# Performance work log

Hardware: AMD Instinct MI355X
Metric: run time of the kernel (lower is better)

## Reference

```python
import jax, jax.numpy as jnp
import numpy as np

NUM_GROUPS = 8
EPS = 1e-5


def group_norm(x, gamma, beta):
    # x: [B, C, H, W], groups over channel dim
    b, c, h, w = x.shape
    xg = x.reshape(b, NUM_GROUPS, c // NUM_GROUPS, h, w)
    mean = xg.mean(axis=(2, 3, 4), keepdims=True)
    var = xg.var(axis=(2, 3, 4), keepdims=True)
    xg = (xg - mean) * jax.lax.rsqrt(var + EPS)
    x = xg.reshape(b, c, h, w)
    return x * gamma[None, :, None, None] + beta[None, :, None, None]


def conv1x1(x, w, bias):
    # 1x1 conv == per-pixel linear: [B,C,H,W] x [O,C] -> [B,O,H,W]
    return jnp.einsum('bchw,oc->bohw', x, w) + bias[None, :, None, None]


def setup_inputs() -> dict:
    key = jax.random.key(0)
    ks = jax.random.split(key, 6)
    B, C, H, W = 16, 512, 32, 32
    s = 1.0 / np.sqrt(C)  # conv2d default init scale-ish
    return {
        'x': jax.random.normal(ks[0], (B, C, H, W), jnp.float32),
        'gn_w': jnp.ones((C,), jnp.float32),
        'gn_b': jnp.zeros((C,), jnp.float32),
        'wq': jax.random.normal(ks[1], (C, C), jnp.float32) * s,
        'bq': jnp.zeros((C,), jnp.float32),
        'wk': jax.random.normal(ks[2], (C, C), jnp.float32) * s,
        'bk': jnp.zeros((C,), jnp.float32),
        'wv': jax.random.normal(ks[3], (C, C), jnp.float32) * s,
        'bv': jnp.zeros((C,), jnp.float32),
        'wo': jax.random.normal(ks[4], (C, C), jnp.float32) * s,
        'bo': jnp.zeros((C,), jnp.float32),
    }


def reference(x, gn_w, gn_b, wq, bq, wk, bk, wv, bv, wo, bo):
    b, c, h, w = x.shape
    scale = c ** (-0.5)
    hn = group_norm(x, gn_w, gn_b)
    q = conv1x1(hn, wq, bq).reshape(b, c, h * w).transpose(0, 2, 1)  # [B, N, C]
    k = conv1x1(hn, wk, bk).reshape(b, c, h * w).transpose(0, 2, 1)  # [B, N, C]
    v = conv1x1(hn, wv, bv).reshape(b, c, h * w).transpose(0, 2, 1)  # [B, N, C]
    attn = jnp.einsum('bnc,bmc->bnm', q, k) * scale                 # [B, N, N]
    attn = jax.nn.softmax(attn, axis=-1)
    out = jnp.einsum('bnm,bmc->bnc', attn, v)                       # [B, N, C]
    out = out.transpose(0, 2, 1).reshape(b, c, h, w)
    out = conv1x1(out, wo, bo)
    return x + out
```

## Files before the change

### kernel.cpp

```cpp
#include <hip/hip_runtime.h>
#include <stdint.h>

#define C_DIM 512
#define HW_N  1024
#define CPG   64
#define EPS_GN 1e-5f
#define SCALE_QK 0.044194173824159216f

typedef __attribute__((ext_vector_type(8))) __bf16 bf16x8v;
typedef __attribute__((ext_vector_type(4))) float  f32x4;

typedef __attribute__((address_space(1))) void gvoid_t;
typedef __attribute__((address_space(3))) void lvoid_t;

__device__ __forceinline__ void gload_lds16(const void* g, void* l) {
  __builtin_amdgcn_global_load_lds((gvoid_t*)g, (lvoid_t*)l, 16, 0, 0);
}

__device__ __forceinline__ uint16_t f2bfbits(float f) {
  __bf16 h = (__bf16)f;
  return __builtin_bit_cast(uint16_t, h);
}

__device__ __forceinline__ float bf2f(uint16_t u) {
  return __builtin_bit_cast(float, (uint32_t)u << 16);
}

template<int N>
__device__ __forceinline__ void vm_wait() {
  if constexpr (N == 0) asm volatile("s_waitcnt vmcnt(0)" ::: "memory");
  else if constexpr (N == 3) asm volatile("s_waitcnt vmcnt(3)" ::: "memory");
  else asm volatile("s_waitcnt vmcnt(4)" ::: "memory");
}

__global__ __launch_bounds__(256)
void gn_stats(const float* __restrict__ x, float2* __restrict__ part)
{
  const int lin  = blockIdx.x;
  const int b    = lin >> 4;
  const int g    = (lin >> 1) & 7;
  const int half = lin & 1;
  const int t    = threadIdx.x;

  const float4* xv = (const float4*)(x + ((long long)(b * C_DIM + g * CPG)) * HW_N
                                       + half * 512);
  float s1 = 0.f, s2 = 0.f;
  for (int i = t; i < 64 * 128; i += 256) {
    const int c  = i >> 7;
    const int nf = i & 127;
    float4 v = xv[c * 256 + nf];
    s1 += v.x + v.y + v.z + v.w;
    s2 += v.x * v.x + v.y * v.y + v.z * v.z + v.w * v.w;
  }
  #pragma unroll
  for (int off = 32; off; off >>= 1) {
    s1 += __shfl_xor(s1, off);
    s2 += __shfl_xor(s2, off);
  }
  __shared__ float red[2][4];
  const int w = t >> 6, l = t & 63;
  if (l == 0) { red[0][w] = s1; red[1][w] = s2; }
  __syncthreads();
  if (t == 0) {
    s1 = red[0][0] + red[0][1] + red[0][2] + red[0][3];
    s2 = red[1][0] + red[1][1] + red[1][2] + red[1][3];
    part[lin] = make_float2(s1, s2);
  }
}

__global__ __launch_bounds__(512)
void gn_norm(const float* __restrict__ x, const float2* __restrict__ part,
             const float* __restrict__ gnw, const float* __restrict__ gnb,
             __bf16* __restrict__ hn)
{
  const int b  = blockIdx.x >> 4;
  const int nc = blockIdx.x & 15;
  const int t  = threadIdx.x;

  __shared__ float asc[512], bsc[512];
  __shared__ float tile[64][65];

  {
    const int c = t;
    const int g = c >> 6;
    float2 p0 = part[(b * 8 + g) * 2 + 0];
    float2 p1 = part[(b * 8 + g) * 2 + 1];
    const float mean = (p0.x + p1.x) * (1.f / 65536.f);
    const float var  = (p0.y + p1.y) * (1.f / 65536.f) - mean * mean;
    const float rstd = rsqrtf(var + EPS_GN);
    const float a = rstd * gnw[c];
    asc[c] = a;
    bsc[c] = gnb[c] - mean * a;
  }
  __syncthreads();

  const long long xb = (long long)b * C_DIM * HW_N + nc * 64;
  __bf16* ob = hn + ((long long)b * HW_N + nc * 64) * C_DIM;

  for (int cg = 0; cg < 8; ++cg) {
    #pragma unroll
    for (int pass = 0; pass < 2; ++pass) {
      const int task = pass * 512 + t;
      const int c  = task >> 4;
      const int f4 = task & 15;
      float4 v = *(const float4*)(x + xb + (long long)(cg * 64 + c) * HW_N + f4 * 4);
      const float a  = asc[cg * 64 + c];
      const float bb = bsc[cg * 64 + c];
      tile[c][f4 * 4 + 0] = v.x * a + bb;
      tile[c][f4 * 4 + 1] = v.y * a + bb;
      tile[c][f4 * 4 + 2] = v.z * a + bb;
      tile[c][f4 * 4 + 3] = v.w * a + bb;
    }
    __syncthreads();
    {
      const int n  = t >> 3;
      const int gc = t & 7;
      uint32_t p[4];
      #pragma unroll
      for (int j = 0; j < 4; ++j) {
        const float f0 = tile[gc * 8 + 2 * j + 0][n];
        const float f1 = tile[gc * 8 + 2 * j + 1][n];
        p[j] = (uint32_t)f2bfbits(f0) | ((uint32_t)f2bfbits(f1) << 16);
      }
      *(uint4*)(ob + (long long)n * C_DIM + cg * 64 + gc * 8) =
          make_uint4(p[0], p[1], p[2], p[3]);
    }
    __syncthreads();
  }
}

__global__ __launch_bounds__(256)
void prep_kernel(const float* __restrict__ wq, const float* __restrict__ wk,
                 const float* __restrict__ wv, const float* __restrict__ wo,
                 const float* __restrict__ bq, const float* __restrict__ bk,
                 __bf16* __restrict__ wqkb, __bf16* __restrict__ wvb,
                 __bf16* __restrict__ wob, float* __restrict__ bqk)
{
  const int blk = blockIdx.x;
  if (blk < 1024) {
    const int which = blk >> 8;
    const int i = (blk & 255) * 256 + threadIdx.x;
    const float* src = (which == 0) ? wq : (which == 1) ? wk : (which == 2) ? wv : wo;
    __bf16* dst = (which == 0) ? wqkb
               : (which == 1) ? (wqkb + (size_t)C_DIM * C_DIM)
               : (which == 2) ? wvb : wob;
    const float scale = (which == 0) ? SCALE_QK : 1.f;
    float4 v = ((const float4*)src)[i];
    uint32_t lo = (uint32_t)f2bfbits(v.x * scale) | ((uint32_t)f2bfbits(v.y * scale) << 16);
    uint32_t hi = (uint32_t)f2bfbits(v.z * scale) | ((uint32_t)f2bfbits(v.w * scale) << 16);
    ((uint2*)dst)[i] = make_uint2(lo, hi);
  } else {
    for (int j = threadIdx.x; j < 1024; j += 256)
      bqk[j] = (j < 512) ? bq[j] * SCALE_QK : bk[j - 512];
  }
}

__global__ __launch_bounds__(256)
void softmax_kernel(__bf16* __restrict__ S)
{
  const long long row = blockIdx.x;
  uint2* sp = (uint2*)(S + row * HW_N);
  const int t = threadIdx.x;
  uint2 raw = sp[t];
  float v0 = bf2f((uint16_t)(raw.x & 0xffff));
  float v1 = bf2f((uint16_t)(raw.x >> 16));
  float v2 = bf2f((uint16_t)(raw.y & 0xffff));
  float v3 = bf2f((uint16_t)(raw.y >> 16));
  float m = fmaxf(fmaxf(v0, v1), fmaxf(v2, v3));
  #pragma unroll
  for (int off = 32; off; off >>= 1) m = fmaxf(m, __shfl_xor(m, off));
  __shared__ float redm[4];
  __shared__ float reds[4];
  const int w = t >> 6, l = t & 63;
  if (l == 0) redm[w] = m;
  __syncthreads();
  m = fmaxf(fmaxf(redm[0], redm[1]), fmaxf(redm[2], redm[3]));
  float e0 = __expf(v0 - m), e1 = __expf(v1 - m);
  float e2 = __expf(v2 - m), e3 = __expf(v3 - m);
  float sum = e0 + e1 + e2 + e3;
  #pragma unroll
  for (int off = 32; off; off >>= 1) sum += __shfl_xor(sum, off);
  if (l == 0) reds[w] = sum;
  __syncthreads();
  sum = reds[0] + reds[1] + reds[2] + reds[3];
  const float inv = 1.f / sum;
  uint32_t lo = (uint32_t)f2bfbits(e0 * inv) | ((uint32_t)f2bfbits(e1 * inv) << 16);
  uint32_t hi = (uint32_t)f2bfbits(e2 * inv) | ((uint32_t)f2bfbits(e3 * inv) << 16);
  sp[t] = make_uint2(lo, hi);
}

template<int BM, int OUTM, int BIASM>
__global__ __launch_bounds__(512, 2)
void gemm8(const __bf16* __restrict__ Amat, const __bf16* __restrict__ Bmat,
           void* __restrict__ Cmat,
           const float* __restrict__ bias,
           const float* __restrict__ resid,
           int lda, int ldb, int ldc,
           long long aS, long long bS, long long cS, int K)
{
  constexpr int TILE_B = BM * 64 + 16384;
  constexpr int CA = BM / 128;
  constexpr int CH = CA + 2;
  constexpr int FPR = BM / 32;
  constexpr int FPP = FPR / 2;

  __shared__ alignas(16) char lds[3 * TILE_B];

  const int tt = threadIdx.x;
  const int w  = tt >> 6;
  const int l  = tt & 63;
  const int lr = l & 15;
  const int lg = l >> 4;
  const int wm = w >> 2;
  const int wn = w & 3;
  const int b  = blockIdx.z;
  const int n0 = blockIdx.x * 256;
  const int m0 = blockIdx.y * BM;

  const __bf16* Ab = Amat + (long long)b * aS;
  const __bf16* Bb = Bmat + (long long)b * bS;

  const int srow = tt >> 2;
  const int sgr  = (tt & 3) ^ ((tt >> 3) & 3);

  f32x4 acc[FPR][4];
  #pragma unroll
  for (int f = 0; f < FPR; ++f)
    #pragma unroll
    for (int c = 0; c < 4; ++c)
      acc[f][c] = (f32x4){0.f, 0.f, 0.f, 0.f};

  auto stage = [&](int t, int c) {
    const int k0 = t << 5;
    char* dst = lds + (t % 3) * TILE_B + c * 8192 + w * 1024;
    const __bf16* src;
    if (c < CA) src = Ab + (long long)(m0 + c * 128 + srow) * lda + k0 + sgr * 8;
    else        src = Bb + (long long)(n0 + (c - CA) * 128 + srow) * ldb + k0 + sgr * 8;
    gload_lds16(src, dst);
  };
  auto rdA = [&](const char* base, int f) -> bf16x8v {
    const int row = wm * (BM / 2) + f * 16 + lr;
    return *(const bf16x8v*)(base + row * 64 + ((lg ^ ((row >> 1) & 3)) << 4));
  };
  auto rdB = [&](const char* base, int c) -> bf16x8v {
    const int row = wn * 64 + c * 16 + lr;
    return *(const bf16x8v*)(base + BM * 64 + row * 64 + ((lg ^ ((row >> 1) & 3)) << 4));
  };

  const int NT = K >> 5;

  #pragma unroll
  for (int c = 0; c < CH; ++c) stage(0, c);
  #pragma unroll
  for (int c = 0; c < CH; ++c) stage(1, c);

  for (int t = 0; t < NT; ++t) {
    const char* buf = lds + (t % 3) * TILE_B;
    if (t + 1 < NT) vm_wait<CH>();
    else            vm_wait<0>();
    __builtin_amdgcn_s_barrier();
    __builtin_amdgcn_sched_barrier(0);

    bf16x8v Bf[4];
    #pragma unroll
    for (int c = 0; c < 4; ++c) Bf[c] = rdB(buf, c);
    bf16x8v Af[FPP];
    #pragma unroll
    for (int f = 0; f < FPP; ++f) Af[f] = rdA(buf, f);
    if (t + 2 < NT) { stage(t + 2, 0); stage(t + 2, 1); }
    asm volatile("s_waitcnt lgkmcnt(0)" ::: "memory");
    __builtin_amdgcn_sched_barrier(0);
    __builtin_amdgcn_s_setprio(1);
    #pragma unroll
    for (int f = 0; f < FPP; ++f)
      #pragma unroll
      for (int c = 0; c < 4; ++c)
        acc[f][c] = __builtin_amdgcn_mfma_f32_16x16x32_bf16(Af[f], Bf[c], acc[f][c], 0, 0, 0);
    __builtin_amdgcn_s_setprio(0);
    __builtin_amdgcn_s_barrier();
    __builtin_amdgcn_sched_barrier(0);

    bf16x8v Ag[FPP];
    #pragma unroll
    for (int f = 0; f < FPP; ++f) Ag[f] = rdA(buf, FPP + f);
    if (t + 2 < NT) {
      #pragma unroll
      for (int c = 2; c < CH; ++c) stage(t + 2, c);
    }
    asm volatile("s_waitcnt lgkmcnt(0)" ::: "memory");
    __builtin_amdgcn_sched_barrier(0);
    __builtin_amdgcn_s_setprio(1);
    #pragma unroll
    for (int f = 0; f < FPP; ++f)
      #pragma unroll
      for (int c = 0; c < 4; ++c)
        acc[FPP + f][c] = __builtin_amdgcn_mfma_f32_16x16x32_bf16(Ag[f], Bf[c], acc[FPP + f][c], 0, 0, 0);
    __builtin_amdgcn_s_setprio(0);
    __builtin_amdgcn_s_barrier();
    __builtin_amdgcn_sched_barrier(0);
  }

  #pragma unroll
  for (int f = 0; f < FPR; ++f) {
    const int rrb = m0 + wm * (BM / 2) + f * 16 + lg * 4;
    #pragma unroll
    for (int c = 0; c < 4; ++c) {
      const int cc = n0 + wn * 64 + c * 16 + lr;
      const float cbias = (BIASM == 1) ? bias[cc] : 0.f;
      #pragma unroll
      for (int r = 0; r < 4; ++r) {
        const int rr = rrb + r;
        float v = acc[f][c][r];
        if (BIASM == 1) v += cbias;
        if (BIASM == 2) v += bias[rr];
        const long long idx = (long long)rr * ldc + cc;
        if (OUTM == 0) {
          ((__bf16*)Cmat + (long long)b * cS)[idx] = (__bf16)v;
        } else if (OUTM == 2) {
          ((float*)Cmat + (long long)b * cS)[idx] = v;
        } else {
          float* Cf = (float*)Cmat + (long long)b * cS;
          const float* Rf = resid + (long long)b * cS;
          Cf[idx] = v + Rf[idx];
        }
      }
    }
  }
}

extern "C" void kernel_launch(void* const* d_in, const int* in_sizes, int n_in,
                              void* d_out, int out_size, void* d_ws, size_t ws_size,
                              hipStream_t stream)
{
  const float* x   = (const float*)d_in[0];
  const float* gnw = (const float*)d_in[1];
  const float* gnb = (const float*)d_in[2];
  const float* wq  = (const float*)d_in[3];
  const float* bq  = (const float*)d_in[4];
  const float* wk  = (const float*)d_in[5];
  const float* bk  = (const float*)d_in[6];
  const float* wv  = (const float*)d_in[7];
  const float* bv  = (const float*)d_in[8];
  const float* wo  = (const float*)d_in[9];
  const float* bo  = (const float*)d_in[10];
  (void)in_sizes; (void)n_in; (void)out_size; (void)ws_size;

  size_t used = 0;
  char* base = (char*)d_ws;
  auto carve = [&](size_t bytes) -> void* {
    used = (used + 255) & ~(size_t)255;
    void* p = base + used;
    used += bytes;
    return p;
  };

  __bf16* wqkb = (__bf16*)carve((size_t)2 * C_DIM * C_DIM * 2);
  __bf16* wvb  = (__bf16*)carve((size_t)C_DIM * C_DIM * 2);
  __bf16* wob  = (__bf16*)carve((size_t)C_DIM * C_DIM * 2);
  float*  bqk  = (float*) carve((size_t)1024 * 4);
  float2* part = (float2*)carve((size_t)256 * 8);

  __bf16* hn   = (__bf16*)carve((size_t)16 * HW_N * C_DIM * 2);
  __bf16* qkb  = (__bf16*)carve((size_t)16 * HW_N * 1024 * 2);
  __bf16* vtb  = (__bf16*)carve((size_t)16 * C_DIM * HW_N * 2);
  __bf16* o1b  = (__bf16*)carve((size_t)16 * HW_N * C_DIM * 2);
  __bf16* Sb   = (__bf16*)carve((size_t)16 * HW_N * HW_N * 2);

  const long long sNC = (long long)HW_N * C_DIM;
  const long long sNN = (long long)HW_N * 1024;

  prep_kernel<<<dim3(1025), 256, 0, stream>>>(wq, wk, wv, wo, bq, bk,
                                              wqkb, wvb, wob, bqk);
  gn_stats<<<dim3(256), 256, 0, stream>>>(x, part);
  gn_norm<<<dim3(256), 512, 0, stream>>>(x, part, gnw, gnb, hn);

  gemm8<256, 0, 1><<<dim3(4, 4, 16), 512, 0, stream>>>(hn, wqkb, qkb, bqk, nullptr,
      C_DIM, C_DIM, 1024, sNC, 0, sNN, C_DIM);

  gemm8<128, 0, 2><<<dim3(4, 4, 16), 512, 0, stream>>>(wvb, hn, vtb, bv, nullptr,
      C_DIM, C_DIM, HW_N, 0, sNC, sNC, C_DIM);

  gemm8<256, 0, 0><<<dim3(4, 4, 16), 512, 0, stream>>>(qkb, qkb + 512, Sb, nullptr, nullptr,
      1024, 1024, 1024, sNN, sNN, sNN, C_DIM);

  softmax_kernel<<<dim3(16 * 1024), 256, 0, stream>>>(Sb);

  gemm8<128, 0, 0><<<dim3(2, 8, 16), 512, 0, stream>>>(Sb, vtb, o1b,
      nullptr, nullptr, 1024, 1024, C_DIM, sNN, sNC, sNC, HW_N);

  gemm8<128, 1, 2><<<dim3(4, 4, 16), 512, 0, stream>>>(wob, o1b, (float*)d_out, bo, x,
      C_DIM, C_DIM, HW_N, 0, sNC, sNC, C_DIM);
}
```

Baseline: 158.3 us.

## Add 256x256 double-buffered quadrant-pipelined GEMM kernel for bf16-output GEMMs

Adds a new gemm256 kernel that computes a 256x256 output tile per 512-thread block. It uses two LDS buffers of 64 KB each and splits every k-step into four quadrant MFMA phases, with the global-to-LDS stages for the next tiles interleaved between phases. The QK projection, V projection, QK^T scores and attention-times-V GEMMs switch to it, so the V and PV launches become larger tiles on fewer blocks. The goal is more arithmetic intensity and better overlap of loads with MFMA, at the cost of 128 KB LDS per block (occupancy risk) and fewer blocks for two of the GEMMs.

```diff
diff --git a/kernel.cpp b/kernel.cpp
--- a/kernel.cpp
+++ b/kernel.cpp
@@ -28,9 +28,10 @@
 
 template<int N>
 __device__ __forceinline__ void vm_wait() {
-  if constexpr (N == 0) asm volatile("s_waitcnt vmcnt(0)" ::: "memory");
+  if constexpr (N == 0)      asm volatile("s_waitcnt vmcnt(0)" ::: "memory");
   else if constexpr (N == 3) asm volatile("s_waitcnt vmcnt(3)" ::: "memory");
-  else asm volatile("s_waitcnt vmcnt(4)" ::: "memory");
+  else if constexpr (N == 4) asm volatile("s_waitcnt vmcnt(4)" ::: "memory");
+  else if constexpr (N == 6) asm volatile("s_waitcnt vmcnt(6)" ::: "memory");
 }
 
 __global__ __launch_bounds__(256)
@@ -189,6 +190,164 @@
   sp[t] = make_uint2(lo, hi);
 }
 
+#define QMFMA(QA, QB, BREG)                                                    \
+  do {                                                                         \
+    __builtin_amdgcn_s_setprio(1);                                             \
+    _Pragma("unroll")                                                          \
+    for (int f_ = 0; f_ < 4; ++f_)                                             \
+      _Pragma("unroll")                                                        \
+      for (int c_ = 0; c_ < 2; ++c_)                                           \
+        _Pragma("unroll")                                                      \
+        for (int kk_ = 0; kk_ < 2; ++kk_)                                      \
+          acc[QA][QB][f_][c_] = __builtin_amdgcn_mfma_f32_16x16x32_bf16(       \
+              Ar[f_][kk_], BREG[c_][kk_], acc[QA][QB][f_][c_], 0, 0, 0);       \
+    __builtin_amdgcn_s_setprio(0);                                             \
+  } while (0)
+
+#define LGKM0_FENCE()                                                          \
+  asm volatile("s_waitcnt lgkmcnt(0)" ::: "memory");                           \
+  __builtin_amdgcn_sched_barrier(0)
+
+template<int BIASM>
+__global__ __launch_bounds__(512, 2)
+void gemm256(const __bf16* __restrict__ Amat, const __bf16* __restrict__ Bmat,
+             __bf16* __restrict__ Cmat, const float* __restrict__ bias,
+             int lda, int ldb, int ldc,
+             long long aS, long long bS, long long cS, int K)
+{
+  __shared__ alignas(16) char lds[131072];
+
+  const int tt = threadIdx.x;
+  const int w  = tt >> 6;
+  const int l  = tt & 63;
+  const int lr = l & 15;
+  const int lg = l >> 4;
+  const int wm = w >> 2;
+  const int wn = w & 3;
+  const int b  = blockIdx.z;
+  const int n0 = blockIdx.x * 256;
+  const int m0 = blockIdx.y * 256;
+
+  const __bf16* Ab = Amat + (long long)b * aS;
+  const __bf16* Bb = Bmat + (long long)b * bS;
+
+  const int r0  = tt >> 3;
+  const int sg8 = ((tt & 7) ^ ((tt >> 3) & 7)) << 3;
+
+  f32x4 acc[2][2][4][2];
+  #pragma unroll
+  for (int qa = 0; qa < 2; ++qa)
+    #pragma unroll
+    for (int qb = 0; qb < 2; ++qb)
+      #pragma unroll
+      for (int f = 0; f < 4; ++f)
+        #pragma unroll
+        for (int c = 0; c < 2; ++c)
+          acc[qa][qb][f][c] = (f32x4){0.f, 0.f, 0.f, 0.f};
+
+  auto stage = [&](int kt, int h) {
+    char* dst = lds + ((kt & 1) << 16) + (h << 14) + w * 1024;
+    const long long ld = (h < 2) ? lda : ldb;
+    const __bf16* src = ((h < 2) ? Ab + (long long)(m0 + (h & 1) * 128) * lda
+                                 : Bb + (long long)(n0 + (h & 1) * 128) * ldb)
+                        + (long long)kt * 64 + sg8;
+    gload_lds16(src + (long long)r0 * ld, dst);
+    gload_lds16(src + (long long)(r0 + 64) * ld, dst + 8192);
+  };
+  auto rdA = [&](const char* bb, int qa, int f, int kk) -> bf16x8v {
+    const int r = wm * 64 + f * 16 + lr;
+    return *(const bf16x8v*)(bb + (qa << 14) + r * 128
+                             + (((kk * 4 + lg) ^ (r & 7)) << 4));
+  };
+  auto rdB = [&](const char* bb, int qb, int c, int kk) -> bf16x8v {
+    const int r = wn * 32 + c * 16 + lr;
+    return *(const bf16x8v*)(bb + 32768 + (qb << 14) + r * 128
+                             + (((kk * 4 + lg) ^ (r & 7)) << 4));
+  };
+
+  const int NT = K >> 6;
+
+  stage(0, 0); stage(0, 1); stage(0, 2); stage(0, 3);
+  stage(1, 0); stage(1, 2); stage(1, 3);
+  vm_wait<6>();
+  __builtin_amdgcn_s_barrier();
+
+  bf16x8v Ar[4][2], B0r[2][2], B1r[2][2];
+
+  for (int t = 0; t < NT; ++t) {
+    const char* buf = lds + ((t & 1) << 16);
+
+    #pragma unroll
+    for (int f = 0; f < 4; ++f)
+      #pragma unroll
+      for (int kk = 0; kk < 2; ++kk) Ar[f][kk] = rdA(buf, 0, f, kk);
+    #pragma unroll
+    for (int c = 0; c < 2; ++c)
+      #pragma unroll
+      for (int kk = 0; kk < 2; ++kk) B0r[c][kk] = rdB(buf, 0, c, kk);
+    if (t + 1 < NT) stage(t + 1, 1);
+    __builtin_amdgcn_s_barrier();
+    LGKM0_FENCE();
+    QMFMA(0, 0, B0r);
+    __builtin_amdgcn_s_barrier();
+    __builtin_amdgcn_sched_barrier(0);
+
+    #pragma unroll
+    for (int c = 0; c < 2; ++c)
+      #pragma unroll
+      for (int kk = 0; kk < 2; ++kk) B1r[c][kk] = rdB(buf, 1, c, kk);
+    if (t + 2 < NT) stage(t + 2, 0);
+    __builtin_amdgcn_s_barrier();
+    LGKM0_FENCE();
+    QMFMA(0, 1, B1r);
+    __builtin_amdgcn_s_barrier();
+    __builtin_amdgcn_sched_barrier(0);
+
+    #pragma unroll
+    for (int f = 0; f < 4; ++f)
+      #pragma unroll
+      for (int kk = 0; kk < 2; ++kk) Ar[f][kk] = rdA(buf, 1, f, kk);
+    if (t + 2 < NT) stage(t + 2, 2);
+    __builtin_amdgcn_s_barrier();
+    LGKM0_FENCE();
+    QMFMA(1, 1, B1r);
+    __builtin_amdgcn_s_barrier();
+    __builtin_amdgcn_sched_barrier(0);
+
+    if (t + 2 < NT) stage(t + 2, 3);
+    QMFMA(1, 0, B0r);
+    if (t + 2 < NT) vm_wait<6>();
+    else            vm_wait<0>();
+    __builtin_amdgcn_s_barrier();
+    __builtin_amdgcn_sched_barrier(0);
+  }
+
+  __bf16* Cb = Cmat + (long long)b * cS;
+  #pragma unroll
+  for (int qa = 0; qa < 2; ++qa) {
+    #pragma unroll
+    for (int f = 0; f < 4; ++f) {
+      const int rrb = m0 + qa * 128 + wm * 64 + f * 16 + lg * 4;
+      #pragma unroll
+      for (int qb = 0; qb < 2; ++qb) {
+        #pragma unroll
+        for (int c = 0; c < 2; ++c) {
+          const int cc = n0 + qb * 128 + wn * 32 + c * 16 + lr;
+          const float cbias = (BIASM == 1) ? bias[cc] : 0.f;
+          #pragma unroll
+          for (int r = 0; r < 4; ++r) {
+            const int rr = rrb + r;
+            float v = acc[qa][qb][f][c][r];
+            if (BIASM == 1) v += cbias;
+            if (BIASM == 2) v += bias[rr];
+            Cb[(long long)rr * ldc + cc] = (__bf16)v;
+          }
+        }
+      }
+    }
+  }
+}
+
 template<int BM, int OUTM, int BIASM>
 __global__ __launch_bounds__(512, 2)
 void gemm8(const __bf16* __restrict__ Amat, const __bf16* __restrict__ Bmat,
@@ -268,8 +427,7 @@
     #pragma unroll
     for (int f = 0; f < FPP; ++f) Af[f] = rdA(buf, f);
     if (t + 2 < NT) { stage(t + 2, 0); stage(t + 2, 1); }
-    asm volatile("s_waitcnt lgkmcnt(0)" ::: "memory");
-    __builtin_amdgcn_sched_barrier(0);
+    LGKM0_FENCE();
     __builtin_amdgcn_s_setprio(1);
     #pragma unroll
     for (int f = 0; f < FPP; ++f)
@@ -287,8 +445,7 @@
       #pragma unroll
       for (int c = 2; c < CH; ++c) stage(t + 2, c);
     }
-    asm volatile("s_waitcnt lgkmcnt(0)" ::: "memory");
-    __builtin_amdgcn_sched_barrier(0);
+    LGKM0_FENCE();
     __builtin_amdgcn_s_setprio(1);
     #pragma unroll
     for (int f = 0; f < FPP; ++f)
@@ -374,19 +531,19 @@
   gn_stats<<<dim3(256), 256, 0, stream>>>(x, part);
   gn_norm<<<dim3(256), 512, 0, stream>>>(x, part, gnw, gnb, hn);
 
-  gemm8<256, 0, 1><<<dim3(4, 4, 16), 512, 0, stream>>>(hn, wqkb, qkb, bqk, nullptr,
+  gemm256<1><<<dim3(4, 4, 16), 512, 0, stream>>>(hn, wqkb, qkb, bqk,
       C_DIM, C_DIM, 1024, sNC, 0, sNN, C_DIM);
 
-  gemm8<128, 0, 2><<<dim3(4, 4, 16), 512, 0, stream>>>(wvb, hn, vtb, bv, nullptr,
+  gemm256<2><<<dim3(4, 2, 16), 512, 0, stream>>>(wvb, hn, vtb, bv,
       C_DIM, C_DIM, HW_N, 0, sNC, sNC, C_DIM);
 
-  gemm8<256, 0, 0><<<dim3(4, 4, 16), 512, 0, stream>>>(qkb, qkb + 512, Sb, nullptr, nullptr,
+  gemm256<0><<<dim3(4, 4, 16), 512, 0, stream>>>(qkb, qkb + 512, Sb, nullptr,
       1024, 1024, 1024, sNN, sNN, sNN, C_DIM);
 
   softmax_kernel<<<dim3(16 * 1024), 256, 0, stream>>>(Sb);
 
-  gemm8<128, 0, 0><<<dim3(2, 8, 16), 512, 0, stream>>>(Sb, vtb, o1b,
-      nullptr, nullptr, 1024, 1024, C_DIM, sNN, sNC, sNC, HW_N);
+  gemm256<0><<<dim3(2, 4, 16), 512, 0, stream>>>(Sb, vtb, o1b, nullptr,
+      1024, 1024, C_DIM, sNN, sNC, sNC, HW_N);
 
   gemm8<128, 1, 2><<<dim3(4, 4, 16), 512, 0, stream>>>(wob, o1b, (float*)d_out, bo, x,
       C_DIM, C_DIM, HW_N, 0, sNC, sNC, C_DIM);
```

New measurement: 168.7 us. 6.6% more time.

## Remap GEMM blocks across XCDs and shrink QK tiles to 128 rows

Applied to the files above, without the earlier changes.

Replaces the 3D grid with a flat 1D grid whose block ids are decoded so that consecutive logical tiles land on the same XCD, which should improve L2 reuse of shared A/B panels. It also moves the QK projection and QK^T GEMMs from BM=256 to BM=128 tiles, doubling the block count to 512 for better CU occupancy. The cost is a smaller per-block tile with less register reuse, plus extra integer decode work. The decode assumes the grid size is divisible by 8.

```diff
diff --git a/kernel.cpp b/kernel.cpp
--- a/kernel.cpp
+++ b/kernel.cpp
@@ -28,9 +28,27 @@
 
 template<int N>
 __device__ __forceinline__ void vm_wait() {
-  if constexpr (N == 0) asm volatile("s_waitcnt vmcnt(0)" ::: "memory");
+  if constexpr (N == 0)      asm volatile("s_waitcnt vmcnt(0)" ::: "memory");
   else if constexpr (N == 3) asm volatile("s_waitcnt vmcnt(3)" ::: "memory");
-  else asm volatile("s_waitcnt vmcnt(4)" ::: "memory");
+  else if constexpr (N == 4) asm volatile("s_waitcnt vmcnt(4)" ::: "memory");
+  else if constexpr (N == 6) asm volatile("s_waitcnt vmcnt(6)" ::: "memory");
+}
+
+#define LGKM0_FENCE()                                                          \
+  asm volatile("s_waitcnt lgkmcnt(0)" ::: "memory");                           \
+  __builtin_amdgcn_sched_barrier(0)
+
+struct BlkId { int bx, by, bz; };
+__device__ __forceinline__ BlkId xcd_decode(int gx, int gy) {
+  const int nwg = gridDim.x;
+  const int bid = blockIdx.x;
+  const int wg  = (bid & 7) * (nwg >> 3) + (bid >> 3);
+  const int pb  = gx * gy;
+  const int bz  = wg / pb;
+  const int rem = wg - bz * pb;
+  const int by  = rem / gx;
+  const int bx  = rem - by * gx;
+  return {bx, by, bz};
 }
 
 __global__ __launch_bounds__(256)
@@ -196,7 +214,7 @@
            const float* __restrict__ bias,
            const float* __restrict__ resid,
            int lda, int ldb, int ldc,
-           long long aS, long long bS, long long cS, int K)
+           long long aS, long long bS, long long cS, int K, int gx, int gy)
 {
   constexpr int TILE_B = BM * 64 + 16384;
   constexpr int CA = BM / 128;
@@ -213,9 +231,10 @@
   const int lg = l >> 4;
   const int wm = w >> 2;
   const int wn = w & 3;
-  const int b  = blockIdx.z;
-  const int n0 = blockIdx.x * 256;
-  const int m0 = blockIdx.y * BM;
+  const BlkId bk_ = xcd_decode(gx, gy);
+  const int b  = bk_.bz;
+  const int n0 = bk_.bx * 256;
+  const int m0 = bk_.by * BM;
 
   const __bf16* Ab = Amat + (long long)b * aS;
   const __bf16* Bb = Bmat + (long long)b * bS;
@@ -268,8 +287,7 @@
     #pragma unroll
     for (int f = 0; f < FPP; ++f) Af[f] = rdA(buf, f);
     if (t + 2 < NT) { stage(t + 2, 0); stage(t + 2, 1); }
-    asm volatile("s_waitcnt lgkmcnt(0)" ::: "memory");
-    __builtin_amdgcn_sched_barrier(0);
+    LGKM0_FENCE();
     __builtin_amdgcn_s_setprio(1);
     #pragma unroll
     for (int f = 0; f < FPP; ++f)
@@ -287,8 +305,7 @@
       #pragma unroll
       for (int c = 2; c < CH; ++c) stage(t + 2, c);
     }
-    asm volatile("s_waitcnt lgkmcnt(0)" ::: "memory");
-    __builtin_amdgcn_sched_barrier(0);
+    LGKM0_FENCE();
     __builtin_amdgcn_s_setprio(1);
     #pragma unroll
     for (int f = 0; f < FPP; ++f)
@@ -374,20 +391,20 @@
   gn_stats<<<dim3(256), 256, 0, stream>>>(x, part);
   gn_norm<<<dim3(256), 512, 0, stream>>>(x, part, gnw, gnb, hn);
 
-  gemm8<256, 0, 1><<<dim3(4, 4, 16), 512, 0, stream>>>(hn, wqkb, qkb, bqk, nullptr,
-      C_DIM, C_DIM, 1024, sNC, 0, sNN, C_DIM);
-
-  gemm8<128, 0, 2><<<dim3(4, 4, 16), 512, 0, stream>>>(wvb, hn, vtb, bv, nullptr,
-      C_DIM, C_DIM, HW_N, 0, sNC, sNC, C_DIM);
-
-  gemm8<256, 0, 0><<<dim3(4, 4, 16), 512, 0, stream>>>(qkb, qkb + 512, Sb, nullptr, nullptr,
-      1024, 1024, 1024, sNN, sNN, sNN, C_DIM);
+  gemm8<128, 0, 1><<<dim3(512), 512, 0, stream>>>(hn, wqkb, qkb, bqk, nullptr,
+      C_DIM, C_DIM, 1024, sNC, 0, sNN, C_DIM, 4, 8);
+
+  gemm8<128, 0, 2><<<dim3(256), 512, 0, stream>>>(wvb, hn, vtb, bv, nullptr,
+      C_DIM, C_DIM, HW_N, 0, sNC, sNC, C_DIM, 4, 4);
+
+  gemm8<128, 0, 0><<<dim3(512), 512, 0, stream>>>(qkb, qkb + 512, Sb, nullptr, nullptr,
+      1024, 1024, 1024, sNN, sNN, sNN, C_DIM, 4, 8);
 
   softmax_kernel<<<dim3(16 * 1024), 256, 0, stream>>>(Sb);
 
-  gemm8<128, 0, 0><<<dim3(2, 8, 16), 512, 0, stream>>>(Sb, vtb, o1b,
-      nullptr, nullptr, 1024, 1024, C_DIM, sNN, sNC, sNC, HW_N);
-
-  gemm8<128, 1, 2><<<dim3(4, 4, 16), 512, 0, stream>>>(wob, o1b, (float*)d_out, bo, x,
-      C_DIM, C_DIM, HW_N, 0, sNC, sNC, C_DIM);
-}
+  gemm8<128, 0, 0><<<dim3(256), 512, 0, stream>>>(Sb, vtb, o1b, nullptr, nullptr,
+      1024, 1024, C_DIM, sNN, sNC, sNC, HW_N, 2, 8);
+
+  gemm8<128, 1, 2><<<dim3(256), 512, 0, stream>>>(wob, o1b, (float*)d_out, bo, x,
+      C_DIM, C_DIM, HW_N, 0, sNC, sNC, C_DIM, 4, 4);
+}
```

After: 149.6 us. 5.5% less time.
